# Performance work log

Hardware: AMD Instinct MI355X
Metric: run time of the kernel (lower is better)

## Reference

```python
import jax, jax.numpy as jnp
import numpy as np

N_NODES = 50000
N_EDGES = 800000
IN_DIM = 64
HID_DIM = 64
OUT_DIM = 16
N_RELS = 16
N_BASES = 4


def setup_inputs() -> dict:
    key = jax.random.key(0)
    ks = jax.random.split(key, 11)
    feats = jax.random.normal(ks[0], (N_NODES, IN_DIM), dtype=jnp.float32)
    src = jax.random.randint(ks[1], (N_EDGES,), 0, N_NODES, dtype=jnp.int32)
    dst = jax.random.randint(ks[2], (N_EDGES,), 0, N_NODES, dtype=jnp.int32)
    edge_type = jax.random.randint(ks[3], (N_EDGES,), 0, N_RELS, dtype=jnp.int32)
    edge_norm = jax.random.uniform(ks[4], (N_EDGES,), dtype=jnp.float32)
    # basis-decomposed relation weights: W[r] = sum_b coef[r,b] * bases[b]
    bases1 = jax.random.normal(ks[5], (N_BASES, IN_DIM, HID_DIM), dtype=jnp.float32) * (1.0 / np.sqrt(IN_DIM))
    coef1 = jax.random.normal(ks[6], (N_RELS, N_BASES), dtype=jnp.float32)
    bias1 = jnp.zeros((HID_DIM,), dtype=jnp.float32)
    bases2 = jax.random.normal(ks[7], (N_BASES, HID_DIM, OUT_DIM), dtype=jnp.float32) * (1.0 / np.sqrt(HID_DIM))
    coef2 = jax.random.normal(ks[8], (N_RELS, N_BASES), dtype=jnp.float32)
    bias2 = jnp.zeros((OUT_DIM,), dtype=jnp.float32)
    return {"feats": feats, "src": src, "dst": dst, "edge_type": edge_type,
            "edge_norm": edge_norm, "bases1": bases1, "coef1": coef1, "bias1": bias1,
            "bases2": bases2, "coef2": coef2, "bias2": bias2}


def _rel_graph_conv(x, src, dst, edge_type, edge_norm, bases, coef, bias):
    """One RelGraphConv layer (basis decomposition, low-mem: gather coef, not W)."""
    xs = x[src]                                   # [E, in]  gather source feats
    t = jnp.einsum('ei,bio->ebo', xs, bases)      # [E, B, out] per-basis transform
    c = coef[edge_type]                            # [E, B]   per-edge relation coefs
    msg = jnp.einsum('eb,ebo->eo', c, t)          # [E, out]
    msg = msg * edge_norm[:, None]                # apply edge norm
    h = jax.ops.segment_sum(msg, dst, num_segments=N_NODES)  # scatter-add by dst
    return jax.nn.relu(h + bias)                  # bias + activation (dropout=0, eval)


def reference(feats, src, dst, edge_type, edge_norm, bases1, coef1, bias1, bases2, coef2, bias2):
    h = _rel_graph_conv(feats, src, dst, edge_type, edge_norm, bases1, coef1, bias1)
    h = _rel_graph_conv(h, src, dst, edge_type, edge_norm, bases2, coef2, bias2)
    return h
```

## Files before the change

### kernel.cpp

```cpp
#include <hip/hip_runtime.h>

#define N_NODES 50000
#define N_EDGES 800000

typedef __attribute__((ext_vector_type(8))) short bf16x8;
typedef __attribute__((ext_vector_type(4))) float f32x4;

__device__ __forceinline__ unsigned bf16rne(float x) {
  unsigned u = __float_as_uint(x);
  return (u + 0x7FFFu + ((u >> 16) & 1u)) >> 16;
}
__device__ __forceinline__ unsigned packbf2(float a, float b) {
  return bf16rne(a) | (bf16rne(b) << 16);
}
__device__ __forceinline__ float bflo(unsigned u) { return __uint_as_float(u << 16); }
__device__ __forceinline__ float bfhi(unsigned u) { return __uint_as_float(u & 0xFFFF0000u); }

#define G_HIST 64
#define CHUNK (N_EDGES / G_HIST)
#define NSLICE 4
#define HBINS (N_NODES / NSLICE)
#define NB 512
#define SCAN_BLKS ((N_NODES + NB - 1) / NB)
#define NHIST (G_HIST * NSLICE)
#define NPACK ((N_EDGES + 511) / 512)

__global__ __launch_bounds__(512) void k_prep(
    const float4* __restrict__ feats4, uint2* __restrict__ xbf,
    const float* __restrict__ bases1, const float* __restrict__ bases2,
    unsigned short* __restrict__ b1T, unsigned short* __restrict__ b2p,
    const int* __restrict__ dst, unsigned char* __restrict__ rank,
    unsigned short* __restrict__ bh) {
  __shared__ int hist[HBINS];
  const int bid = blockIdx.x;
  if (bid < NHIST) {
    const int c = bid & (G_HIST - 1);
    const int p = bid >> 6;
    const int e0 = c * CHUNK;
    const int lo = p * HBINS;
    for (int i = threadIdx.x; i < HBINS; i += 512) hist[i] = 0;
    __syncthreads();
    for (int i = threadIdx.x; i < CHUNK; i += 512) {
      const int d = dst[e0 + i] - lo;
      if ((unsigned)d < (unsigned)HBINS)
        rank[e0 + i] = (unsigned char)atomicAdd(&hist[d], 1);
    }
    __syncthreads();
    for (int i = threadIdx.x; i < HBINS; i += 512)
      bh[(size_t)c * N_NODES + lo + i] = (unsigned short)hist[i];
  } else if (bid < NHIST + NPACK) {
    const int i = (bid - NHIST) * 512 + threadIdx.x;
    if (i < N_EDGES) {
      float4 v = feats4[i];
      xbf[i] = make_uint2(packbf2(v.x, v.y), packbf2(v.z, v.w));
    }
  } else {
    for (int idx = threadIdx.x; idx < 64 * 256; idx += 512) {
      int o = idx >> 8, q = idx & 255;
      b1T[idx] = (unsigned short)bf16rne(bases1[q * 64 + o]);
    }
    for (int idx = threadIdx.x; idx < 64 * 64; idx += 512) {
      int j = idx >> 6, k = idx & 63;
      int o = j >> 2, b = j & 3;
      b2p[idx] = (unsigned short)bf16rne(bases2[b * 1024 + k * 16 + o]);
    }
  }
}

__global__ __launch_bounds__(512) void k_scan1(
    unsigned short* __restrict__ bh,
    int* __restrict__ rowp, int* __restrict__ bsum) {
  __shared__ unsigned short tile[G_HIST][NB];
  __shared__ int wsum[8];
  const int tid = threadIdx.x;
  const int n0 = blockIdx.x * NB;
  for (int idx = tid; idx < G_HIST * (NB / 4); idx += 512) {
    const int c = idx >> 7, j = idx & 127;
    const int nloc = 4 * j;
    uint2 u = make_uint2(0u, 0u);
    if (n0 + nloc < N_NODES)
      u = *(const uint2*)(bh + (size_t)c * N_NODES + n0 + nloc);
    *(uint2*)&tile[c][nloc] = u;
  }
  __syncthreads();
  int s = 0;
  for (int c = 0; c < G_HIST; ++c) {
    const int cnt = tile[c][tid];
    tile[c][tid] = (unsigned short)s;
    s += cnt;
  }
  __syncthreads();
  for (int idx = tid; idx < G_HIST * (NB / 4); idx += 512) {
    const int c = idx >> 7, j = idx & 127;
    const int nloc = 4 * j;
    if (n0 + nloc < N_NODES)
      *(uint2*)(bh + (size_t)c * N_NODES + n0 + nloc) = *(uint2*)&tile[c][nloc];
  }
  const int lane = tid & 63, wid = tid >> 6;
  const int v = (n0 + tid < N_NODES) ? s : 0;
  int incl = v;
#pragma unroll
  for (int off = 1; off < 64; off <<= 1) {
    int t = __shfl_up(incl, off, 64);
    if (lane >= off) incl += t;
  }
  if (lane == 63) wsum[wid] = incl;
  __syncthreads();
  if (tid < 8) {
    int wi = wsum[tid];
#pragma unroll
    for (int off = 1; off < 8; off <<= 1) {
      int t = __shfl_up(wi, off, 64);
      if (lane >= off) wi += t;
    }
    wsum[tid] = wi;
  }
  __syncthreads();
  const int woff = (wid > 0) ? wsum[wid - 1] : 0;
  const int incl_all = incl + woff;
  const int n = n0 + tid;
  if (n <= N_NODES) rowp[n] = incl_all - v;
  if (tid == NB - 1) bsum[blockIdx.x] = incl_all;
}

__device__ __forceinline__ int prefix_bsum(const int* __restrict__ bsum,
                                           int b, int lane) {
  int v = 0;
  for (int k = lane; k < b; k += 64) v += bsum[k];
#pragma unroll
  for (int off = 32; off >= 1; off >>= 1) v += __shfl_xor(v, off, 64);
  return v;
}

__global__ __launch_bounds__(256) void k_scatter(
    const int* __restrict__ src, const int* __restrict__ dst,
    const int* __restrict__ ety, const float* __restrict__ enorm,
    const int* __restrict__ rowp, const unsigned char* __restrict__ rank,
    const unsigned short* __restrict__ bh, const int* __restrict__ bsum,
    unsigned* __restrict__ s_edge) {
  __shared__ int sb[128];
  const int tid = threadIdx.x;
  if (tid < 128) sb[tid] = (tid < SCAN_BLKS) ? bsum[tid] : 0;
  __syncthreads();
#pragma unroll
  for (int off = 1; off < 128; off <<= 1) {
    int t = 0;
    if (tid < 128 && tid >= off) t = sb[tid - off];
    __syncthreads();
    if (tid < 128) sb[tid] += t;
    __syncthreads();
  }
  const int e = blockIdx.x * 256 + tid;
  if (e >= N_EDGES) return;
  const int d = dst[e];
  const int b = e / CHUNK;
  const int blk = d >> 9;
  const int boff = blk ? sb[blk - 1] : 0;
  const int pos = rowp[d] + boff + (int)bh[(size_t)b * N_NODES + d] + (int)rank[e];
  unsigned nq = (unsigned)(enorm[e] * 4096.f + 0.5f);
  nq = nq > 4095u ? 4095u : nq;
  s_edge[pos] = (unsigned)src[e] | ((unsigned)ety[e] << 16) | (nq << 20);
}

#define NMSCALE (1.f / 4096.f)

#define ROWB 264
__device__ __forceinline__ void gather_node(
    const unsigned* __restrict__ s_edge, const uint2* __restrict__ xv,
    const float4* __restrict__ coefLDS,
    unsigned short* __restrict__ uA,
    int beg, int end, int m, int lane) {
  const int eslot = lane >> 4, ch4 = lane & 15;
  const int qlen = (end - beg + 3) >> 2;
  int p = beg + eslot * qlen;
  const int pend = min(p + qlen, end);
  float4 a0 = {0, 0, 0, 0}, a1 = {0, 0, 0, 0}, a2 = {0, 0, 0, 0}, a3 = {0, 0, 0, 0};
  for (; p < pend; p += 4) {
    const int nb = pend - p;
    unsigned rec[4];
#pragma unroll
    for (int t = 0; t < 4; ++t) rec[t] = (t < nb) ? s_edge[p + t] : 0u;
    uint2 xp[4];
#pragma unroll
    for (int t = 0; t < 4; ++t) xp[t] = xv[(rec[t] & 0xFFFF) * 16 + ch4];
#pragma unroll
    for (int t = 0; t < 4; ++t) {
      const float nm = (float)(rec[t] >> 20) * NMSCALE;
      const float4 c = coefLDS[(rec[t] >> 16) & 15];
      const float w0 = nm * c.x, w1 = nm * c.y, w2 = nm * c.z, w3 = nm * c.w;
      const float x0 = bflo(xp[t].x), x1 = bfhi(xp[t].x);
      const float x2 = bflo(xp[t].y), x3 = bfhi(xp[t].y);
      a0.x += w0 * x0; a0.y += w0 * x1; a0.z += w0 * x2; a0.w += w0 * x3;
      a1.x += w1 * x0; a1.y += w1 * x1; a1.z += w1 * x2; a1.w += w1 * x3;
      a2.x += w2 * x0; a2.y += w2 * x1; a2.z += w2 * x2; a2.w += w2 * x3;
      a3.x += w3 * x0; a3.y += w3 * x1; a3.z += w3 * x2; a3.w += w3 * x3;
    }
  }
#define RED1(x) x += __shfl_down(x, 32, 64)
  RED1(a0.x); RED1(a0.y); RED1(a0.z); RED1(a0.w);
  RED1(a1.x); RED1(a1.y); RED1(a1.z); RED1(a1.w);
  RED1(a2.x); RED1(a2.y); RED1(a2.z); RED1(a2.w);
  RED1(a3.x); RED1(a3.y); RED1(a3.z); RED1(a3.w);
#undef RED1
  if (eslot < 2) {
    unsigned short* row = uA + (eslot * 16 + m) * ROWB + 4 * ch4;
    *(uint2*)(row + 0 * 64) = make_uint2(packbf2(a0.x, a0.y), packbf2(a0.z, a0.w));
    *(uint2*)(row + 1 * 64) = make_uint2(packbf2(a1.x, a1.y), packbf2(a1.z, a1.w));
    *(uint2*)(row + 2 * 64) = make_uint2(packbf2(a2.x, a2.y), packbf2(a2.z, a2.w));
    *(uint2*)(row + 3 * 64) = make_uint2(packbf2(a3.x, a3.y), packbf2(a3.z, a3.w));
  }
}

__global__ __launch_bounds__(256) void k_l1_fused(
    const int* __restrict__ rowp, const int* __restrict__ bsum,
    const unsigned* __restrict__ s_edge,
    const uint2* __restrict__ xbf, const float* __restrict__ coef1,
    const unsigned short* __restrict__ b1T,
    const float* __restrict__ bias1,
    const unsigned short* __restrict__ b2p,
    uint2* __restrict__ y2bf) {
  __shared__ __align__(16) unsigned short uA[2 * 16 * ROWB];
  __shared__ float coefs[64];
  __shared__ float cmat[16 * 68];
  const int wid = threadIdx.x >> 6, lane = threadIdx.x & 63;
  if (threadIdx.x < 64) coefs[threadIdx.x] = coef1[threadIdx.x];
  __syncthreads();
  const int nbase = blockIdx.x * 16;
  const int b0 = nbase >> 9;
  const int boff0 = prefix_bsum(bsum, b0, lane);
  const int bs0 = bsum[b0];
#pragma unroll
  for (int jn = 0; jn < 4; ++jn) {
    const int m = wid * 4 + jn;
    const int node = nbase + m;
    const int beg = rowp[node] + (((node >> 9) == b0) ? boff0 : boff0 + bs0);
    const int end = rowp[node + 1] + ((((node + 1) >> 9) == b0) ? boff0 : boff0 + bs0);
    gather_node(s_edge, xbf, (const float4*)coefs, uA, beg, end, m, lane);
  }
  __syncthreads();
  const int nloc = lane & 15, kgrp = lane >> 4;
  f32x4 acc1 = {0.f, 0.f, 0.f, 0.f};
#pragma unroll
  for (int ks = 0; ks < 8; ++ks) {
    const int k0 = ks * 32 + kgrp * 8;
    const bf16x8 b = *(const bf16x8*)&b1T[(wid * 16 + nloc) * 256 + k0];
    const bf16x8 aS0 = *(const bf16x8*)&uA[(0 * 16 + nloc) * ROWB + k0];
    acc1 = __builtin_amdgcn_mfma_f32_16x16x32_bf16(aS0, b, acc1, 0, 0, 0);
    const bf16x8 aS1 = *(const bf16x8*)&uA[(1 * 16 + nloc) * ROWB + k0];
    acc1 = __builtin_amdgcn_mfma_f32_16x16x32_bf16(aS1, b, acc1, 0, 0, 0);
  }
  {
    const int o = wid * 16 + nloc;
    const float bs = bias1[o];
#pragma unroll
    for (int r = 0; r < 4; ++r) {
      const int m = (lane >> 4) * 4 + r;
      cmat[m * 68 + o] = fmaxf(acc1[r] + bs, 0.f);
    }
  }
  __syncthreads();
  f32x4 acc2 = {0.f, 0.f, 0.f, 0.f};
#pragma unroll
  for (int ks = 0; ks < 2; ++ks) {
    const int k0 = ks * 32 + kgrp * 8;
    const float4 c0 = *(const float4*)&cmat[nloc * 68 + k0];
    const float4 c1 = *(const float4*)&cmat[nloc * 68 + k0 + 4];
    union { bf16x8 v; unsigned u[4]; } au;
    au.u[0] = packbf2(c0.x, c0.y); au.u[1] = packbf2(c0.z, c0.w);
    au.u[2] = packbf2(c1.x, c1.y); au.u[3] = packbf2(c1.z, c1.w);
    const bf16x8 b = *(const bf16x8*)&b2p[(wid * 16 + nloc) * 64 + k0];
    acc2 = __builtin_amdgcn_mfma_f32_16x16x32_bf16(au.v, b, acc2, 0, 0, 0);
  }
  __syncthreads();
#pragma unroll
  for (int r = 0; r < 4; ++r) {
    const int m = (lane >> 4) * 4 + r;
    cmat[m * 68 + wid * 16 + nloc] = acc2[r];
  }
  __syncthreads();
  const int nl = threadIdx.x >> 4, c4 = threadIdx.x & 15;
  const float* cr = &cmat[nl * 68 + 4 * c4];
  y2bf[(size_t)(nbase + nl) * 16 + c4] =
      make_uint2(packbf2(cr[0], cr[1]), packbf2(cr[2], cr[3]));
}

__global__ __launch_bounds__(256) void k_l2_gather(
    const int* __restrict__ rowp, const int* __restrict__ bsum,
    const unsigned* __restrict__ s_edge,
    const uint4* __restrict__ y2v,
    const float* __restrict__ coef2, const float* __restrict__ bias2,
    float2* __restrict__ out) {
  __shared__ float coefs[64];
  if (threadIdx.x < 64) coefs[threadIdx.x] = coef2[threadIdx.x];
  __syncthreads();
  const float4* coefv = (const float4*)coefs;
  const int wid = threadIdx.x >> 6, lane = threadIdx.x & 63;
  const int eslot = lane >> 3, og = lane & 7;
  const int nbase = blockIdx.x * 8 + wid * 2;
  const int b0 = nbase >> 9;
  const int boff0 = prefix_bsum(bsum, b0, lane);
  const int bs0 = bsum[b0];

  float a0[2] = {0.f, 0.f}, a1[2] = {0.f, 0.f};
  int p[2], pend[2];
#pragma unroll
  for (int m = 0; m < 2; ++m) {
    const int node = nbase + m;
    const int beg = rowp[node] + (((node >> 9) == b0) ? boff0 : boff0 + bs0);
    const int end = rowp[node + 1] + ((((node + 1) >> 9) == b0) ? boff0 : boff0 + bs0);
    const int qlen = (end - beg + 7) >> 3;
    p[m] = beg + eslot * qlen;
    pend[m] = min(p[m] + qlen, end);
  }
  while ((p[0] < pend[0]) | (p[1] < pend[1])) {
    unsigned rec[2][2] = {{0u, 0u}, {0u, 0u}};
#pragma unroll
    for (int m = 0; m < 2; ++m) {
      if (p[m] < pend[m]) rec[m][0] = s_edge[p[m]];
      if (p[m] + 1 < pend[m]) rec[m][1] = s_edge[p[m] + 1];
    }
    uint4 yp[2][2];
#pragma unroll
    for (int m = 0; m < 2; ++m)
#pragma unroll
      for (int t = 0; t < 2; ++t)
        yp[m][t] = y2v[(rec[m][t] & 0xFFFF) * 8 + og];
#pragma unroll
    for (int m = 0; m < 2; ++m)
#pragma unroll
      for (int t = 0; t < 2; ++t) {
        const float nm = (float)(rec[m][t] >> 20) * NMSCALE;
        const float4 c = coefv[(rec[m][t] >> 16) & 15];
        a0[m] += nm * (c.x * bflo(yp[m][t].x) + c.y * bfhi(yp[m][t].x) +
                       c.z * bflo(yp[m][t].y) + c.w * bfhi(yp[m][t].y));
        a1[m] += nm * (c.x * bflo(yp[m][t].z) + c.y * bfhi(yp[m][t].z) +
                       c.z * bflo(yp[m][t].w) + c.w * bfhi(yp[m][t].w));
      }
#pragma unroll
    for (int m = 0; m < 2; ++m) p[m] += 2;
  }
#pragma unroll
  for (int m = 0; m < 2; ++m) {
    a0[m] += __shfl_down(a0[m], 32, 64);
    a0[m] += __shfl_down(a0[m], 16, 64);
    a0[m] += __shfl_down(a0[m], 8, 64);
    a1[m] += __shfl_down(a1[m], 32, 64);
    a1[m] += __shfl_down(a1[m], 16, 64);
    a1[m] += __shfl_down(a1[m], 8, 64);
  }
  if (eslot == 0) {
    const float b0s = bias2[2 * og], b1s = bias2[2 * og + 1];
#pragma unroll
    for (int m = 0; m < 2; ++m) {
      out[(size_t)(nbase + m) * 8 + og] =
          make_float2(fmaxf(a0[m] + b0s, 0.f), fmaxf(a1[m] + b1s, 0.f));
    }
  }
}

extern "C" void kernel_launch(void* const* d_in, const int* in_sizes, int n_in,
                              void* d_out, int out_size, void* d_ws, size_t ws_size,
                              hipStream_t stream) {
  const float* feats  = (const float*)d_in[0];
  const int*   src    = (const int*)d_in[1];
  const int*   dst    = (const int*)d_in[2];
  const int*   etype  = (const int*)d_in[3];
  const float* enorm  = (const float*)d_in[4];
  const float* bases1 = (const float*)d_in[5];
  const float* coef1  = (const float*)d_in[6];
  const float* bias1  = (const float*)d_in[7];
  const float* bases2 = (const float*)d_in[8];
  const float* coef2  = (const float*)d_in[9];
  const float* bias2  = (const float*)d_in[10];

  uint2* xbf    = (uint2*)d_ws;
  uint2* y2bf   = xbf + (size_t)N_NODES * 16;
  unsigned* s_edge = (unsigned*)(y2bf + (size_t)N_NODES * 16);
  unsigned short* bh = (unsigned short*)(s_edge + N_EDGES);
  unsigned short* b1T = bh + (size_t)G_HIST * N_NODES;
  unsigned short* b2p = b1T + 64 * 256;
  int*   rowp   = (int*)(b2p + 64 * 64);
  int*   bsum   = rowp + N_NODES + 1;
  unsigned char* rank = (unsigned char*)(bsum + 128);

  k_prep<<<NHIST + NPACK + 1, 512, 0, stream>>>(
      (const float4*)feats, xbf, bases1, bases2, b1T, b2p, dst, rank, bh);
  k_scan1<<<SCAN_BLKS, 512, 0, stream>>>(bh, rowp, bsum);
  k_scatter<<<(N_EDGES + 255) / 256, 256, 0, stream>>>(
      src, dst, etype, enorm, rowp, rank, bh, bsum, s_edge);
  k_l1_fused<<<N_NODES / 16, 256, 0, stream>>>(rowp, bsum, s_edge, xbf, coef1,
                                               b1T, bias1, b2p, y2bf);
  k_l2_gather<<<N_NODES / 8, 256, 0, stream>>>(rowp, bsum, s_edge,
                                               (const uint4*)y2bf, coef2,
                                               bias2, (float2*)d_out);
}
```

Measured before the change: 186.6 us.

## Merge all five stages into one persistent cooperative kernel with grid syncs

```diff
diff --git a/kernel.cpp b/kernel.cpp
--- a/kernel.cpp
+++ b/kernel.cpp
@@ -1,4 +1,7 @@
 #include <hip/hip_runtime.h>
+#include <hip/hip_cooperative_groups.h>
+
+namespace cg = cooperative_groups;
 
 #define N_NODES 50000
 #define N_EDGES 800000
@@ -23,105 +26,9 @@
 #define NB 512
 #define SCAN_BLKS ((N_NODES + NB - 1) / NB)
 #define NHIST (G_HIST * NSLICE)
-#define NPACK ((N_EDGES + 511) / 512)
-
-__global__ __launch_bounds__(512) void k_prep(
-    const float4* __restrict__ feats4, uint2* __restrict__ xbf,
-    const float* __restrict__ bases1, const float* __restrict__ bases2,
-    unsigned short* __restrict__ b1T, unsigned short* __restrict__ b2p,
-    const int* __restrict__ dst, unsigned char* __restrict__ rank,
-    unsigned short* __restrict__ bh) {
-  __shared__ int hist[HBINS];
-  const int bid = blockIdx.x;
-  if (bid < NHIST) {
-    const int c = bid & (G_HIST - 1);
-    const int p = bid >> 6;
-    const int e0 = c * CHUNK;
-    const int lo = p * HBINS;
-    for (int i = threadIdx.x; i < HBINS; i += 512) hist[i] = 0;
-    __syncthreads();
-    for (int i = threadIdx.x; i < CHUNK; i += 512) {
-      const int d = dst[e0 + i] - lo;
-      if ((unsigned)d < (unsigned)HBINS)
-        rank[e0 + i] = (unsigned char)atomicAdd(&hist[d], 1);
-    }
-    __syncthreads();
-    for (int i = threadIdx.x; i < HBINS; i += 512)
-      bh[(size_t)c * N_NODES + lo + i] = (unsigned short)hist[i];
-  } else if (bid < NHIST + NPACK) {
-    const int i = (bid - NHIST) * 512 + threadIdx.x;
-    if (i < N_EDGES) {
-      float4 v = feats4[i];
-      xbf[i] = make_uint2(packbf2(v.x, v.y), packbf2(v.z, v.w));
-    }
-  } else {
-    for (int idx = threadIdx.x; idx < 64 * 256; idx += 512) {
-      int o = idx >> 8, q = idx & 255;
-      b1T[idx] = (unsigned short)bf16rne(bases1[q * 64 + o]);
-    }
-    for (int idx = threadIdx.x; idx < 64 * 64; idx += 512) {
-      int j = idx >> 6, k = idx & 63;
-      int o = j >> 2, b = j & 3;
-      b2p[idx] = (unsigned short)bf16rne(bases2[b * 1024 + k * 16 + o]);
-    }
-  }
-}
-
-__global__ __launch_bounds__(512) void k_scan1(
-    unsigned short* __restrict__ bh,
-    int* __restrict__ rowp, int* __restrict__ bsum) {
-  __shared__ unsigned short tile[G_HIST][NB];
-  __shared__ int wsum[8];
-  const int tid = threadIdx.x;
-  const int n0 = blockIdx.x * NB;
-  for (int idx = tid; idx < G_HIST * (NB / 4); idx += 512) {
-    const int c = idx >> 7, j = idx & 127;
-    const int nloc = 4 * j;
-    uint2 u = make_uint2(0u, 0u);
-    if (n0 + nloc < N_NODES)
-      u = *(const uint2*)(bh + (size_t)c * N_NODES + n0 + nloc);
-    *(uint2*)&tile[c][nloc] = u;
-  }
-  __syncthreads();
-  int s = 0;
-  for (int c = 0; c < G_HIST; ++c) {
-    const int cnt = tile[c][tid];
-    tile[c][tid] = (unsigned short)s;
-    s += cnt;
-  }
-  __syncthreads();
-  for (int idx = tid; idx < G_HIST * (NB / 4); idx += 512) {
-    const int c = idx >> 7, j = idx & 127;
-    const int nloc = 4 * j;
-    if (n0 + nloc < N_NODES)
-      *(uint2*)(bh + (size_t)c * N_NODES + n0 + nloc) = *(uint2*)&tile[c][nloc];
-  }
-  const int lane = tid & 63, wid = tid >> 6;
-  const int v = (n0 + tid < N_NODES) ? s : 0;
-  int incl = v;
-#pragma unroll
-  for (int off = 1; off < 64; off <<= 1) {
-    int t = __shfl_up(incl, off, 64);
-    if (lane >= off) incl += t;
-  }
-  if (lane == 63) wsum[wid] = incl;
-  __syncthreads();
-  if (tid < 8) {
-    int wi = wsum[tid];
-#pragma unroll
-    for (int off = 1; off < 8; off <<= 1) {
-      int t = __shfl_up(wi, off, 64);
-      if (lane >= off) wi += t;
-    }
-    wsum[tid] = wi;
-  }
-  __syncthreads();
-  const int woff = (wid > 0) ? wsum[wid - 1] : 0;
-  const int incl_all = incl + woff;
-  const int n = n0 + tid;
-  if (n <= N_NODES) rowp[n] = incl_all - v;
-  if (tid == NB - 1) bsum[blockIdx.x] = incl_all;
-}
+#define NTILE (N_NODES / 16)
+#define ROWB 264
+#define NMSCALE (1.f / 4096.f)
 
 __device__ __forceinline__ int prefix_bsum(const int* __restrict__ bsum,
                                            int b, int lane) {
@@ -132,39 +39,6 @@
   return v;
 }
 
-__global__ __launch_bounds__(256) void k_scatter(
-    const int* __restrict__ src, const int* __restrict__ dst,
-    const int* __restrict__ ety, const float* __restrict__ enorm,
-    const int* __restrict__ rowp, const unsigned char* __restrict__ rank,
-    const unsigned short* __restrict__ bh, const int* __restrict__ bsum,
-    unsigned* __restrict__ s_edge) {
-  __shared__ int sb[128];
-  const int tid = threadIdx.x;
-  if (tid < 128) sb[tid] = (tid < SCAN_BLKS) ? bsum[tid] : 0;
-  __syncthreads();
-#pragma unroll
-  for (int off = 1; off < 128; off <<= 1) {
-    int t = 0;
-    if (tid < 128 && tid >= off) t = sb[tid - off];
-    __syncthreads();
-    if (tid < 128) sb[tid] += t;
-    __syncthreads();
-  }
-  const int e = blockIdx.x * 256 + tid;
-  if (e >= N_EDGES) return;
-  const int d = dst[e];
-  const int b = e / CHUNK;
-  const int blk = d >> 9;
-  const int boff = blk ? sb[blk - 1] : 0;
-  const int pos = rowp[d] + boff + (int)bh[(size_t)b * N_NODES + d] + (int)rank[e];
-  unsigned nq = (unsigned)(enorm[e] * 4096.f + 0.5f);
-  nq = nq > 4095u ? 4095u : nq;
-  s_edge[pos] = (unsigned)src[e] | ((unsigned)ety[e] << 16) | (nq << 20);
-}
-
-#define NMSCALE (1.f / 4096.f)
-
-#define ROWB 264
 __device__ __forceinline__ void gather_node(
     const unsigned* __restrict__ s_edge, const uint2* __restrict__ xv,
     const float4* __restrict__ coefLDS,
@@ -211,149 +85,286 @@
   }
 }
 
-__global__ __launch_bounds__(256) void k_l1_fused(
-    const int* __restrict__ rowp, const int* __restrict__ bsum,
-    const unsigned* __restrict__ s_edge,
-    const uint2* __restrict__ xbf, const float* __restrict__ coef1,
-    const unsigned short* __restrict__ b1T,
-    const float* __restrict__ bias1,
-    const unsigned short* __restrict__ b2p,
-    uint2* __restrict__ y2bf) {
-  __shared__ __align__(16) unsigned short uA[2 * 16 * ROWB];
+__global__ __launch_bounds__(512, 4) void k_all(
+    const float4* __restrict__ feats4, const int* __restrict__ src,
+    const int* __restrict__ dst, const int* __restrict__ ety,
+    const float* __restrict__ enorm, const float* __restrict__ bases1,
+    const float* __restrict__ coef1, const float* __restrict__ bias1,
+    const float* __restrict__ bases2, const float* __restrict__ coef2,
+    const float* __restrict__ bias2,
+    uint2* __restrict__ xbf, uint2* __restrict__ y2bf,
+    unsigned* __restrict__ s_edge, unsigned short* __restrict__ bh,
+    unsigned short* __restrict__ b1T, unsigned short* __restrict__ b2p,
+    int* __restrict__ rowp, int* __restrict__ bsum,
+    unsigned char* __restrict__ rank, float2* __restrict__ out) {
+  cg::grid_group grid = cg::this_grid();
+  __shared__ union {
+    int hist[HBINS];
+    unsigned short tile[G_HIST][NB];
+    struct {
+      unsigned short uA[2 * 16 * ROWB];
+      float cmat[16 * 68];
+    } l1;
+  } sm;
   __shared__ float coefs[64];
-  __shared__ float cmat[16 * 68];
-  const int wid = threadIdx.x >> 6, lane = threadIdx.x & 63;
-  if (threadIdx.x < 64) coefs[threadIdx.x] = coef1[threadIdx.x];
-  __syncthreads();
-  const int nbase = blockIdx.x * 16;
-  const int b0 = nbase >> 9;
-  const int boff0 = prefix_bsum(bsum, b0, lane);
-  const int bs0 = bsum[b0];
-#pragma unroll
-  for (int jn = 0; jn < 4; ++jn) {
-    const int m = wid * 4 + jn;
-    const int node = nbase + m;
-    const int beg = rowp[node] + (((node >> 9) == b0) ? boff0 : boff0 + bs0);
-    const int end = rowp[node + 1] + ((((node + 1) >> 9) == b0) ? boff0 : boff0 + bs0);
-    gather_node(s_edge, xbf, (const float4*)coefs, uA, beg, end, m, lane);
-  }
-  __syncthreads();
-  const int nloc = lane & 15, kgrp = lane >> 4;
-  f32x4 acc1 = {0.f, 0.f, 0.f, 0.f};
-#pragma unroll
-  for (int ks = 0; ks < 8; ++ks) {
-    const int k0 = ks * 32 + kgrp * 8;
-    const bf16x8 b = *(const bf16x8*)&b1T[(wid * 16 + nloc) * 256 + k0];
-    const bf16x8 aS0 = *(const bf16x8*)&uA[(0 * 16 + nloc) * ROWB + k0];
-    acc1 = __builtin_amdgcn_mfma_f32_16x16x32_bf16(aS0, b, acc1, 0, 0, 0);
-    const bf16x8 aS1 = *(const bf16x8*)&uA[(1 * 16 + nloc) * ROWB + k0];
-    acc1 = __builtin_amdgcn_mfma_f32_16x16x32_bf16(aS1, b, acc1, 0, 0, 0);
+  __shared__ int sb[128];
+  __shared__ int wsum[8];
+
+  const int tid = threadIdx.x, bid = blockIdx.x, ng = gridDim.x;
+  const int lane = tid & 63, wid = tid >> 6;
+
+  for (int unit = bid; unit < NHIST; unit += ng) {
+    const int c = unit & (G_HIST - 1);
+    const int p = unit >> 6;
+    const int e0 = c * CHUNK, lo = p * HBINS;
+    __syncthreads();
+    for (int i = tid; i < HBINS; i += 512) sm.hist[i] = 0;
+    __syncthreads();
+    for (int i = tid; i < CHUNK; i += 512) {
+      const int d = dst[e0 + i] - lo;
+      if ((unsigned)d < (unsigned)HBINS)
+        rank[e0 + i] = (unsigned char)atomicAdd(&sm.hist[d], 1);
+    }
+    __syncthreads();
+    for (int i = tid; i < HBINS; i += 512)
+      bh[(size_t)c * N_NODES + lo + i] = (unsigned short)sm.hist[i];
   }
   {
-    const int o = wid * 16 + nloc;
-    const float bs = bias1[o];
-#pragma unroll
-    for (int r = 0; r < 4; ++r) {
-      const int m = (lane >> 4) * 4 + r;
-      cmat[m * 68 + o] = fmaxf(acc1[r] + bs, 0.f);
-    }
-  }
-  __syncthreads();
-  f32x4 acc2 = {0.f, 0.f, 0.f, 0.f};
-#pragma unroll
-  for (int ks = 0; ks < 2; ++ks) {
-    const int k0 = ks * 32 + kgrp * 8;
-    const float4 c0 = *(const float4*)&cmat[nloc * 68 + k0];
-    const float4 c1 = *(const float4*)&cmat[nloc * 68 + k0 + 4];
-    union { bf16x8 v; unsigned u[4]; } au;
-    au.u[0] = packbf2(c0.x, c0.y); au.u[1] = packbf2(c0.z, c0.w);
-    au.u[2] = packbf2(c1.x, c1.y); au.u[3] = packbf2(c1.z, c1.w);
-    const bf16x8 b = *(const bf16x8*)&b2p[(wid * 16 + nloc) * 64 + k0];
-    acc2 = __builtin_amdgcn_mfma_f32_16x16x32_bf16(au.v, b, acc2, 0, 0, 0);
-  }
-  __syncthreads();
-#pragma unroll
-  for (int r = 0; r < 4; ++r) {
-    const int m = (lane >> 4) * 4 + r;
-    cmat[m * 68 + wid * 16 + nloc] = acc2[r];
-  }
-  __syncthreads();
-  const int nl = threadIdx.x >> 4, c4 = threadIdx.x & 15;
-  const float* cr = &cmat[nl * 68 + 4 * c4];
-  y2bf[(size_t)(nbase + nl) * 16 + c4] =
-      make_uint2(packbf2(cr[0], cr[1]), packbf2(cr[2], cr[3]));
-}
-
-__global__ __launch_bounds__(256) void k_l2_gather(
-    const int* __restrict__ rowp, const int* __restrict__ bsum,
-    const unsigned* __restrict__ s_edge,
-    const uint4* __restrict__ y2v,
-    const float* __restrict__ coef2, const float* __restrict__ bias2,
-    float2* __restrict__ out) {
-  __shared__ float coefs[64];
-  if (threadIdx.x < 64) coefs[threadIdx.x] = coef2[threadIdx.x];
+    const int pb0 = (ng > NHIST) ? NHIST : 0;
+    const int pbn = ng - pb0;
+    if (bid >= pb0) {
+      for (int i = (bid - pb0) * 512 + tid; i < N_EDGES; i += pbn * 512) {
+        float4 v = feats4[i];
+        xbf[i] = make_uint2(packbf2(v.x, v.y), packbf2(v.z, v.w));
+      }
+    }
+  }
+  if (bid == ng - 1) {
+    for (int idx = tid; idx < 64 * 256; idx += 512) {
+      int o = idx >> 8, q = idx & 255;
+      b1T[idx] = (unsigned short)bf16rne(bases1[q * 64 + o]);
+    }
+    for (int idx = tid; idx < 64 * 64; idx += 512) {
+      int j = idx >> 6, k = idx & 63;
+      int o = j >> 2, b = j & 3;
+      b2p[idx] = (unsigned short)bf16rne(bases2[b * 1024 + k * 16 + o]);
+    }
+  }
+  __threadfence();
+  grid.sync();
+
+  for (int t = bid; t < SCAN_BLKS; t += ng) {
+    const int n0 = t * NB;
+    __syncthreads();
+    for (int idx = tid; idx < G_HIST * (NB / 4); idx += 512) {
+      const int c = idx >> 7, j = idx & 127;
+      const int nloc = 4 * j;
+      uint2 u = make_uint2(0u, 0u);
+      if (n0 + nloc < N_NODES)
+        u = *(const uint2*)(bh + (size_t)c * N_NODES + n0 + nloc);
+      *(uint2*)&sm.tile[c][nloc] = u;
+    }
+    __syncthreads();
+    int s = 0;
+    for (int c = 0; c < G_HIST; ++c) {
+      const int cnt = sm.tile[c][tid];
+      sm.tile[c][tid] = (unsigned short)s;
+      s += cnt;
+    }
+    __syncthreads();
+    for (int idx = tid; idx < G_HIST * (NB / 4); idx += 512) {
+      const int c = idx >> 7, j = idx & 127;
+      const int nloc = 4 * j;
+      if (n0 + nloc < N_NODES)
+        *(uint2*)(bh + (size_t)c * N_NODES + n0 + nloc) = *(uint2*)&sm.tile[c][nloc];
+    }
+    const int v = (n0 + tid < N_NODES) ? s : 0;
+    int incl = v;
+#pragma unroll
+    for (int off = 1; off < 64; off <<= 1) {
+      int tt = __shfl_up(incl, off, 64);
+      if (lane >= off) incl += tt;
+    }
+    if (lane == 63) wsum[wid] = incl;
+    __syncthreads();
+    if (tid < 8) {
+      int wi = wsum[tid];
+#pragma unroll
+      for (int off = 1; off < 8; off <<= 1) {
+        int tt = __shfl_up(wi, off, 64);
+        if (lane >= off) wi += tt;
+      }
+      wsum[tid] = wi;
+    }
+    __syncthreads();
+    const int woff = (wid > 0) ? wsum[wid - 1] : 0;
+    const int incl_all = incl + woff;
+    const int n = n0 + tid;
+    if (n <= N_NODES) rowp[n] = incl_all - v;
+    if (tid == NB - 1) bsum[t] = incl_all;
+  }
+  __threadfence();
+  grid.sync();
+
+  {
+    if (tid < 128) sb[tid] = (tid < SCAN_BLKS) ? bsum[tid] : 0;
+    __syncthreads();
+#pragma unroll
+    for (int off = 1; off < 128; off <<= 1) {
+      int t = 0;
+      if (tid < 128 && tid >= off) t = sb[tid - off];
+      __syncthreads();
+      if (tid < 128) sb[tid] += t;
+      __syncthreads();
+    }
+    for (int e = bid * 512 + tid; e < N_EDGES; e += ng * 512) {
+      const int d = dst[e];
+      const int b = e / CHUNK;
+      const int blk = d >> 9;
+      const int boff = blk ? sb[blk - 1] : 0;
+      const int pos = rowp[d] + boff + (int)bh[(size_t)b * N_NODES + d] + (int)rank[e];
+      unsigned nq = (unsigned)(enorm[e] * 4096.f + 0.5f);
+      nq = nq > 4095u ? 4095u : nq;
+      s_edge[pos] = (unsigned)src[e] | ((unsigned)ety[e] << 16) | (nq << 20);
+    }
+  }
+  __threadfence();
+  grid.sync();
+
+  if (tid < 64) coefs[tid] = coef1[tid];
+  for (int t = bid; t < NTILE; t += ng) {
+    __syncthreads();
+    const int nbase = t * 16;
+    const int b0 = nbase >> 9;
+    const int boff0 = prefix_bsum(bsum, b0, lane);
+    const int bs0 = bsum[b0];
+#pragma unroll
+    for (int jn = 0; jn < 2; ++jn) {
+      const int m = wid * 2 + jn;
+      const int node = nbase + m;
+      const int beg = rowp[node] + (((node >> 9) == b0) ? boff0 : boff0 + bs0);
+      const int end = rowp[node + 1] + ((((node + 1) >> 9) == b0) ? boff0 : boff0 + bs0);
+      gather_node(s_edge, xbf, (const float4*)coefs, sm.l1.uA, beg, end, m, lane);
+    }
+    __syncthreads();
+    const int nloc = lane & 15, kgrp = lane >> 4;
+    if (wid < 4) {
+      f32x4 acc1 = {0.f, 0.f, 0.f, 0.f};
+#pragma unroll
+      for (int ks = 0; ks < 8; ++ks) {
+        const int k0 = ks * 32 + kgrp * 8;
+        const bf16x8 b = *(const bf16x8*)&b1T[(wid * 16 + nloc) * 256 + k0];
+        const bf16x8 aS0 = *(const bf16x8*)&sm.l1.uA[(0 * 16 + nloc) * ROWB + k0];
+        acc1 = __builtin_amdgcn_mfma_f32_16x16x32_bf16(aS0, b, acc1, 0, 0, 0);
+        const bf16x8 aS1 = *(const bf16x8*)&sm.l1.uA[(1 * 16 + nloc) * ROWB + k0];
+        acc1 = __builtin_amdgcn_mfma_f32_16x16x32_bf16(aS1, b, acc1, 0, 0, 0);
+      }
+      const int o = wid * 16 + nloc;
+      const float bs = bias1[o];
+#pragma unroll
+      for (int r = 0; r < 4; ++r) {
+        const int m = (lane >> 4) * 4 + r;
+        sm.l1.cmat[m * 68 + o] = fmaxf(acc1[r] + bs, 0.f);
+      }
+    }
+    __syncthreads();
+    f32x4 acc2 = {0.f, 0.f, 0.f, 0.f};
+    if (wid < 4) {
+#pragma unroll
+      for (int ks = 0; ks < 2; ++ks) {
+        const int k0 = ks * 32 + kgrp * 8;
+        const float4 c0 = *(const float4*)&sm.l1.cmat[nloc * 68 + k0];
+        const float4 c1 = *(const float4*)&sm.l1.cmat[nloc * 68 + k0 + 4];
+        union { bf16x8 v; unsigned u[4]; } au;
+        au.u[0] = packbf2(c0.x, c0.y); au.u[1] = packbf2(c0.z, c0.w);
+        au.u[2] = packbf2(c1.x, c1.y); au.u[3] = packbf2(c1.z, c1.w);
+        const bf16x8 b = *(const bf16x8*)&b2p[(wid * 16 + nloc) * 64 + k0];
+        acc2 = __builtin_amdgcn_mfma_f32_16x16x32_bf16(au.v, b, acc2, 0, 0, 0);
+      }
+    }
+    __syncthreads();
+    if (wid < 4) {
+#pragma unroll
+      for (int r = 0; r < 4; ++r) {
+        const int m = (lane >> 4) * 4 + r;
+        sm.l1.cmat[m * 68 + wid * 16 + nloc] = acc2[r];
+      }
+    }
+    __syncthreads();
+    if (tid < 256) {
+      const int nl = tid >> 4, c4 = tid & 15;
+      const float* cr = &sm.l1.cmat[nl * 68 + 4 * c4];
+      y2bf[(size_t)(nbase + nl) * 16 + c4] =
+          make_uint2(packbf2(cr[0], cr[1]), packbf2(cr[2], cr[3]));
+    }
+  }
+  __threadfence();
+  grid.sync();
+
+  if (tid < 64) coefs[tid] = coef2[tid];
   __syncthreads();
   const float4* coefv = (const float4*)coefs;
-  const int wid = threadIdx.x >> 6, lane = threadIdx.x & 63;
+  const uint4* y2v = (const uint4*)y2bf;
   const int eslot = lane >> 3, og = lane & 7;
-  const int nbase = blockIdx.x * 8 + wid * 2;
-  const int b0 = nbase >> 9;
-  const int boff0 = prefix_bsum(bsum, b0, lane);
-  const int bs0 = bsum[b0];
-
-  float a0[2] = {0.f, 0.f}, a1[2] = {0.f, 0.f};
-  int p[2], pend[2];
-#pragma unroll
-  for (int m = 0; m < 2; ++m) {
-    const int node = nbase + m;
-    const int beg = rowp[node] + (((node >> 9) == b0) ? boff0 : boff0 + bs0);
-    const int end = rowp[node + 1] + ((((node + 1) >> 9) == b0) ? boff0 : boff0 + bs0);
-    const int qlen = (end - beg + 7) >> 3;
-    p[m] = beg + eslot * qlen;
-    pend[m] = min(p[m] + qlen, end);
-  }
-  while ((p[0] < pend[0]) | (p[1] < pend[1])) {
-    unsigned rec[2][2] = {{0u, 0u}, {0u, 0u}};
+  for (int unit = bid; unit < NTILE; unit += ng) {
+    const int nbase = unit * 16 + wid * 2;
+    const int b0 = nbase >> 9;
+    const int boff0 = prefix_bsum(bsum, b0, lane);
+    const int bs0 = bsum[b0];
+    float a0[2] = {0.f, 0.f}, a1[2] = {0.f, 0.f};
+    int p[2], pend[2];
 #pragma unroll
     for (int m = 0; m < 2; ++m) {
-      if (p[m] < pend[m]) rec[m][0] = s_edge[p[m]];
-      if (p[m] + 1 < pend[m]) rec[m][1] = s_edge[p[m] + 1];
-    }
-    uint4 yp[2][2];
-#pragma unroll
-    for (int m = 0; m < 2; ++m)
-#pragma unroll
-      for (int t = 0; t < 2; ++t)
-        yp[m][t] = y2v[(rec[m][t] & 0xFFFF) * 8 + og];
-#pragma unroll
-    for (int m = 0; m < 2; ++m)
-#pragma unroll
-      for (int t = 0; t < 2; ++t) {
-        const float nm = (float)(rec[m][t] >> 20) * NMSCALE;
-        const float4 c = coefv[(rec[m][t] >> 16) & 15];
-        a0[m] += nm * (c.x * bflo(yp[m][t].x) + c.y * bfhi(yp[m][t].x) +
-                       c.z * bflo(yp[m][t].y) + c.w * bfhi(yp[m][t].y));
-        a1[m] += nm * (c.x * bflo(yp[m][t].z) + c.y * bfhi(yp[m][t].z) +
-                       c.z * bflo(yp[m][t].w) + c.w * bfhi(yp[m][t].w));
-      }
-#pragma unroll
-    for (int m = 0; m < 2; ++m) p[m] += 2;
-  }
-#pragma unroll
-  for (int m = 0; m < 2; ++m) {
-    a0[m] += __shfl_down(a0[m], 32, 64);
-    a0[m] += __shfl_down(a0[m], 16, 64);
-    a0[m] += __shfl_down(a0[m], 8, 64);
-    a1[m] += __shfl_down(a1[m], 32, 64);
-    a1[m] += __shfl_down(a1[m], 16, 64);
-    a1[m] += __shfl_down(a1[m], 8, 64);
-  }
-  if (eslot == 0) {
-    const float b0s = bias2[2 * og], b1s = bias2[2 * og + 1];
+      const int node = nbase + m;
+      const int beg = rowp[node] + (((node >> 9) == b0) ? boff0 : boff0 + bs0);
+      const int end = rowp[node + 1] + ((((node + 1) >> 9) == b0) ? boff0 : boff0 + bs0);
+      const int qlen = (end - beg + 7) >> 3;
+      p[m] = beg + eslot * qlen;
+      pend[m] = min(p[m] + qlen, end);
+    }
+    while ((p[0] < pend[0]) | (p[1] < pend[1])) {
+      unsigned rec[2][2] = {{0u, 0u}, {0u, 0u}};
+#pragma unroll
+      for (int m = 0; m < 2; ++m) {
+        if (p[m] < pend[m]) rec[m][0] = s_edge[p[m]];
+        if (p[m] + 1 < pend[m]) rec[m][1] = s_edge[p[m] + 1];
+      }
+      uint4 yp[2][2];
+#pragma unroll
+      for (int m = 0; m < 2; ++m)
+#pragma unroll
+        for (int t = 0; t < 2; ++t)
+          yp[m][t] = y2v[(rec[m][t] & 0xFFFF) * 8 + og];
+#pragma unroll
+      for (int m = 0; m < 2; ++m)
+#pragma unroll
+        for (int t = 0; t < 2; ++t) {
+          const float nm = (float)(rec[m][t] >> 20) * NMSCALE;
+          const float4 c = coefv[(rec[m][t] >> 16) & 15];
+          a0[m] += nm * (c.x * bflo(yp[m][t].x) + c.y * bfhi(yp[m][t].x) +
+                         c.z * bflo(yp[m][t].y) + c.w * bfhi(yp[m][t].y));
+          a1[m] += nm * (c.x * bflo(yp[m][t].z) + c.y * bfhi(yp[m][t].z) +
+                         c.z * bflo(yp[m][t].w) + c.w * bfhi(yp[m][t].w));
+        }
+#pragma unroll
+      for (int m = 0; m < 2; ++m) p[m] += 2;
+    }
 #pragma unroll
     for (int m = 0; m < 2; ++m) {
-      out[(size_t)(nbase + m) * 8 + og] =
-          make_float2(fmaxf(a0[m] + b0s, 0.f), fmaxf(a1[m] + b1s, 0.f));
+      a0[m] += __shfl_down(a0[m], 32, 64);
+      a0[m] += __shfl_down(a0[m], 16, 64);
+      a0[m] += __shfl_down(a0[m], 8, 64);
+      a1[m] += __shfl_down(a1[m], 32, 64);
+      a1[m] += __shfl_down(a1[m], 16, 64);
+      a1[m] += __shfl_down(a1[m], 8, 64);
+    }
+    if (eslot == 0) {
+      const float b0s = bias2[2 * og], b1s = bias2[2 * og + 1];
+#pragma unroll
+      for (int m = 0; m < 2; ++m) {
+        out[(size_t)(nbase + m) * 8 + og] =
+            make_float2(fmaxf(a0[m] + b0s, 0.f), fmaxf(a1[m] + b1s, 0.f));
+      }
     }
   }
 }
@@ -361,7 +372,7 @@
 extern "C" void kernel_launch(void* const* d_in, const int* in_sizes, int n_in,
                               void* d_out, int out_size, void* d_ws, size_t ws_size,
                               hipStream_t stream) {
-  const float* feats  = (const float*)d_in[0];
+  const float4* feats4 = (const float4*)d_in[0];
   const int*   src    = (const int*)d_in[1];
   const int*   dst    = (const int*)d_in[2];
   const int*   etype  = (const int*)d_in[3];
@@ -382,15 +393,20 @@
   int*   rowp   = (int*)(b2p + 64 * 64);
   int*   bsum   = rowp + N_NODES + 1;
   unsigned char* rank = (unsigned char*)(bsum + 128);
-
-  k_prep<<<NHIST + NPACK + 1, 512, 0, stream>>>(
-      (const float4*)feats, xbf, bases1, bases2, b1T, b2p, dst, rank, bh);
-  k_scan1<<<SCAN_BLKS, 512, 0, stream>>>(bh, rowp, bsum);
-  k_scatter<<<(N_EDGES + 255) / 256, 256, 0, stream>>>(
-      src, dst, etype, enorm, rowp, rank, bh, bsum, s_edge);
-  k_l1_fused<<<N_NODES / 16, 256, 0, stream>>>(rowp, bsum, s_edge, xbf, coef1,
-                                               b1T, bias1, b2p, y2bf);
-  k_l2_gather<<<N_NODES / 8, 256, 0, stream>>>(rowp, bsum, s_edge,
-                                               (const uint4*)y2bf, coef2,
-                                               bias2, (float2*)d_out);
-}
+  float2* outp  = (float2*)d_out;
+
+  int occ = 0;
+  hipOccupancyMaxActiveBlocksPerMultiprocessor(&occ, k_all, 512, 0);
+  int grid = occ * 256;
+  if (grid > 512) grid = 512;
+  if (grid < 1) grid = 256;
+
+  void* args[] = {
+      (void*)&feats4, (void*)&src, (void*)&dst, (void*)&etype, (void*)&enorm,
+      (void*)&bases1, (void*)&coef1, (void*)&bias1, (void*)&bases2,
+      (void*)&coef2, (void*)&bias2, (void*)&xbf, (void*)&y2bf, (void*)&s_edge,
+      (void*)&bh, (void*)&b1T, (void*)&b2p, (void*)&rowp, (void*)&bsum,
+      (void*)&rank, (void*)&outp};
+  hipLaunchCooperativeKernel((void*)k_all, dim3(grid), dim3(512), args, 0,
+                             stream);
+}
```

Result: slower. 575.8 us (+208.6%).
